# Optimization experiments

Measured on AMD Instinct MI355X. Metric: run time of the kernel, lower is better.

The kernel has to match this reference:

```python
import jax, jax.numpy as jnp
import numpy as np

DIM = 512
HEADS = 16
GRID = (32, 32)
MLP_HIDDEN = 2048
EPS = 1e-5


def _relative_position_index(hw):
    H, W = hw
    coords = np.stack(np.meshgrid(np.arange(H), np.arange(W), indexing='ij'))  # [2,H,W]
    coords = coords.reshape(2, -1)  # [2, L]
    rel = coords[:, :, None] - coords[:, None, :]  # [2, L, L]
    rel = rel.transpose(1, 2, 0).astype(np.int64)  # [L, L, 2]
    rel[:, :, 0] += H - 1
    rel[:, :, 1] += W - 1
    rel[:, :, 0] *= 2 * W - 1
    return jnp.asarray(rel.sum(-1))  # [L, L]


def setup_inputs() -> dict:
    key = jax.random.key(0)
    ks = jax.random.split(key, 12)
    L = GRID[0] * GRID[1]
    table_size = (2 * GRID[0] - 1) * (2 * GRID[1] - 1)
    s = 0.02
    return {
        'x': jax.random.normal(ks[0], (8, L, DIM), jnp.float32),
        'rel_index': _relative_position_index(GRID),
        'bias_table': s * jax.random.truncated_normal(ks[1], -2.0, 2.0, (table_size, HEADS), jnp.float32),
        'qkv_w': jax.random.normal(ks[2], (DIM, 3 * DIM), jnp.float32) / np.sqrt(DIM),
        'qkv_b': jnp.zeros((3 * DIM,), jnp.float32),
        'proj_w': jax.random.normal(ks[3], (DIM, DIM), jnp.float32) / np.sqrt(DIM),
        'proj_b': jnp.zeros((DIM,), jnp.float32),
        'n1_g': jnp.ones((DIM,), jnp.float32),
        'n1_b': jnp.zeros((DIM,), jnp.float32),
        'n2_g': jnp.ones((DIM,), jnp.float32),
        'n2_b': jnp.zeros((DIM,), jnp.float32),
        'fc1_w': jax.random.normal(ks[4], (DIM, MLP_HIDDEN), jnp.float32) / np.sqrt(DIM),
        'fc1_b': jnp.zeros((MLP_HIDDEN,), jnp.float32),
        'fc2_w': jax.random.normal(ks[5], (MLP_HIDDEN, DIM), jnp.float32) / np.sqrt(MLP_HIDDEN),
        'fc2_b': jnp.zeros((DIM,), jnp.float32),
    }


def _layernorm(x, g, b):
    mu = jnp.mean(x, -1, keepdims=True)
    var = jnp.mean(jnp.square(x - mu), -1, keepdims=True)
    return (x - mu) * jax.lax.rsqrt(var + EPS) * g + b


def reference(x, rel_index, bias_table, qkv_w, qkv_b, proj_w, proj_b,
              n1_g, n1_b, n2_g, n2_b, fc1_w, fc1_b, fc2_w, fc2_b):
    B, L, C = x.shape
    hd = C // HEADS
    scale = hd ** -0.5

    h = _layernorm(x, n1_g, n1_b)
    qkv = (h @ qkv_w + qkv_b).reshape(B, L, 3, HEADS, hd)
    qkv = jnp.transpose(qkv, (2, 0, 3, 1, 4))  # [3, B, H, L, hd]
    q, k, v = qkv[0] * scale, qkv[1], qkv[2]

    attn = jnp.einsum('bhld,bhmd->bhlm', q, k)  # [B, H, L, L]
    bias = bias_table[rel_index]                # [L, L, H]
    attn = attn + jnp.transpose(bias, (2, 0, 1))[None]
    attn = jax.nn.softmax(attn, axis=-1)

    out = jnp.einsum('bhlm,bhmd->bhld', attn, v)
    out = jnp.transpose(out, (0, 2, 1, 3)).reshape(B, L, C)
    out = out @ proj_w + proj_b

    x = x + out
    h2 = _layernorm(x, n2_g, n2_b)
    mlp = jax.nn.gelu(h2 @ fc1_w + fc1_b, approximate=False) @ fc2_w + fc2_b
    return x + mlp
```

## Files before the change

### kernel.cpp

```cpp
#include <hip/hip_runtime.h>

typedef unsigned short u16;
typedef __attribute__((ext_vector_type(8))) short bf16x8;
typedef __attribute__((ext_vector_type(4))) float f32x4;

__device__ __forceinline__ float bf2f(unsigned int u) {
    union { unsigned int i; float f; } c; c.i = u << 16; return c.f;
}
__device__ __forceinline__ unsigned int f2bf(float f) {
    union { float f; unsigned int i; } c; c.f = f;
    unsigned int x = c.i;
    unsigned int r = x + 0x7FFFu + ((x >> 16) & 1u);
    return r >> 16;
}

__device__ __forceinline__ void gload_lds16(const u16* g, u16* l) {
    __builtin_amdgcn_global_load_lds(
        (__attribute__((address_space(1))) void*)const_cast<u16*>(g),
        (__attribute__((address_space(3))) void*)l,
        16, 0, 0);
}

__global__ __launch_bounds__(256) void wconv_kernel(const float* __restrict__ W,
                                                    u16* __restrict__ Wt, int K, int N) {
    __shared__ u16 tile[32][36];
    int k0 = blockIdx.y * 32, n0 = blockIdx.x * 32;
    int t = threadIdx.x;
    int r = t >> 3, c4 = (t & 7) * 4;
    float4 v = *(const float4*)(W + (size_t)(k0 + r) * N + n0 + c4);
    tile[r][c4 + 0] = (u16)f2bf(v.x);
    tile[r][c4 + 1] = (u16)f2bf(v.y);
    tile[r][c4 + 2] = (u16)f2bf(v.z);
    tile[r][c4 + 3] = (u16)f2bf(v.w);
    __syncthreads();
    int n = t >> 3, k4 = (t & 7) * 4;
    u16 a0 = tile[k4 + 0][n], a1 = tile[k4 + 1][n];
    u16 a2 = tile[k4 + 2][n], a3 = tile[k4 + 3][n];
    uint2 st;
    st.x = (unsigned)a0 | ((unsigned)a1 << 16);
    st.y = (unsigned)a2 | ((unsigned)a3 << 16);
    *(uint2*)(Wt + (size_t)(n0 + n) * K + k0 + k4) = st;
}

__global__ __launch_bounds__(256) void ln_kernel(const float* __restrict__ x,
                                                 const float* __restrict__ g,
                                                 const float* __restrict__ b,
                                                 u16* __restrict__ y) {
    int row = blockIdx.x * 4 + (threadIdx.x >> 6);
    int t = threadIdx.x & 63;
    const float* xr = x + (size_t)row * 512 + t * 8;
    float4 a = *(const float4*)xr;
    float4 c = *(const float4*)(xr + 4);
    float v[8] = { a.x, a.y, a.z, a.w, c.x, c.y, c.z, c.w };
    float s = 0.f, ss = 0.f;
#pragma unroll
    for (int i = 0; i < 8; ++i) { s += v[i]; ss += v[i] * v[i]; }
#pragma unroll
    for (int off = 32; off; off >>= 1) {
        s  += __shfl_down(s, off);
        ss += __shfl_down(ss, off);
    }
    s = __shfl(s, 0); ss = __shfl(ss, 0);
    float mu = s * (1.0f / 512.0f);
    float var = ss * (1.0f / 512.0f) - mu * mu;
    float r = rsqrtf(var + 1e-5f);
    float4 g0 = *(const float4*)(g + t * 8);
    float4 g1 = *(const float4*)(g + t * 8 + 4);
    float4 b0 = *(const float4*)(b + t * 8);
    float4 b1 = *(const float4*)(b + t * 8 + 4);
    float gv[8] = { g0.x, g0.y, g0.z, g0.w, g1.x, g1.y, g1.z, g1.w };
    float bv[8] = { b0.x, b0.y, b0.z, b0.w, b1.x, b1.y, b1.z, b1.w };
    unsigned int o[4];
#pragma unroll
    for (int i = 0; i < 4; ++i) {
        float o0 = (v[2 * i] - mu) * r * gv[2 * i] + bv[2 * i];
        float o1 = (v[2 * i + 1] - mu) * r * gv[2 * i + 1] + bv[2 * i + 1];
        o[i] = f2bf(o0) | (f2bf(o1) << 16);
    }
    *(uint4*)(y + (size_t)row * 512 + t * 8) = make_uint4(o[0], o[1], o[2], o[3]);
}

template <int ACT, int RES, int COUT>
__global__ __launch_bounds__(256) void gemm_mfma(const u16* __restrict__ A, int lda,
                                                 const u16* __restrict__ Bt,
                                                 const float* __restrict__ bias,
                                                 const float* __restrict__ res, int ldres,
                                                 void* __restrict__ C, int ldC, int K,
                                                 int gx) {
    __shared__ u16 As[2][2][64 * 32];
    __shared__ u16 Bs[2][2][128 * 32];
    int tid = threadIdx.x;
    int G = gridDim.x;
    int bid = blockIdx.x;
    int wg = (bid & 7) * (G >> 3) + (bid >> 3);
    int bm = (wg / gx) * 64, bn = (wg % gx) * 128;
    int lane = tid & 63, wv = tid >> 6;
    int q = lane >> 4, lr = lane & 15;
    int wr = wv >> 1, wc = wv & 1;

    const u16* Ag = A + (size_t)(bm + wv * 16 + (lane >> 2)) * lda + (lane & 3) * 8;
    const u16* Bg = Bt + (size_t)(bn + wv * 32 + (lane >> 2)) * K + (lane & 3) * 8;
    int aoff  = (wv * 16) * 32;
    int boff0 = (wv * 32) * 32;
    int boff1 = (wv * 32 + 16) * 32;
    int apf = (wr * 32 + lr) * 32 + q * 8;
    int bpf = (wc * 64 + lr) * 32 + q * 8;

    f32x4 acc[2][4];
#pragma unroll
    for (int i = 0; i < 2; ++i)
#pragma unroll
        for (int j = 0; j < 4; ++j) acc[i][j] = (f32x4){0.f, 0.f, 0.f, 0.f};

#pragma unroll
    for (int p = 0; p < 2; ++p) {
        gload_lds16(Ag + p * 32, &As[0][p][aoff]);
        gload_lds16(Bg + p * 32, &Bs[0][p][boff0]);
        gload_lds16(Bg + (size_t)16 * K + p * 32, &Bs[0][p][boff1]);
    }
    __syncthreads();

    int cur = 0;
    for (int k0 = 0; k0 < K; k0 += 64) {
        int nxt = cur ^ 1;
        if (k0 + 64 < K) {
#pragma unroll
            for (int p = 0; p < 2; ++p) {
                gload_lds16(Ag + k0 + 64 + p * 32, &As[nxt][p][aoff]);
                gload_lds16(Bg + k0 + 64 + p * 32, &Bs[nxt][p][boff0]);
                gload_lds16(Bg + (size_t)16 * K + k0 + 64 + p * 32, &Bs[nxt][p][boff1]);
            }
        }
#pragma unroll
        for (int p = 0; p < 2; ++p) {
            bf16x8 af[2], bfr[4];
#pragma unroll
            for (int i = 0; i < 2; ++i) af[i] = *(const bf16x8*)&As[cur][p][apf + i * 16 * 32];
#pragma unroll
            for (int j = 0; j < 4; ++j) bfr[j] = *(const bf16x8*)&Bs[cur][p][bpf + j * 16 * 32];
#pragma unroll
            for (int i = 0; i < 2; ++i)
#pragma unroll
                for (int j = 0; j < 4; ++j)
                    acc[i][j] = __builtin_amdgcn_mfma_f32_16x16x32_bf16(af[i], bfr[j], acc[i][j], 0, 0, 0);
        }
        __syncthreads();
        cur = nxt;
    }

    float bv[4];
#pragma unroll
    for (int j = 0; j < 4; ++j)
        bv[j] = bias ? bias[bn + wc * 64 + j * 16 + lr] : 0.f;
#pragma unroll
    for (int i = 0; i < 2; ++i) {
#pragma unroll
        for (int j = 0; j < 4; ++j) {
            int col = bn + wc * 64 + j * 16 + lr;
#pragma unroll
            for (int r = 0; r < 4; ++r) {
                int row = bm + wr * 32 + i * 16 + q * 4 + r;
                float v = acc[i][j][r] + bv[j];
                if (ACT) v = 0.5f * v * (1.0f + erff(v * 0.7071067811865475f));
                if (RES) v += res[(size_t)row * ldres + col];
                if (COUT == 0) ((u16*)C)[(size_t)row * ldC + col] = (u16)f2bf(v);
                else           ((float*)C)[(size_t)row * ldC + col] = v;
            }
        }
    }
}

__global__ __launch_bounds__(256) void attn_mfma(u16* __restrict__ qkv,
                                                 const float* __restrict__ bias_table) {
    __shared__ u16 Ks[128][40];
    __shared__ u16 Vt[32][136];
    __shared__ u16 Ps[4][16][136];
    __shared__ float biasc[3969];
    int tid = threadIdx.x;
    int bid = blockIdx.x;
    int grp = (bid & 7) * 8 + ((bid >> 3) >> 4);
    int qt = (bid >> 3) & 15;
    int h = grp & 15, z = grp >> 4;
    u16* qkvz = qkv + (size_t)z * 1024 * 1536;

    for (int i = tid; i < 3969; i += 256) biasc[i] = bias_table[(size_t)i * 16 + h];

    int lane = tid & 63, wv = tid >> 6;
    int q = lane >> 4, m = lane & 15;

    int qrow = qt * 64 + wv * 16 + m;
    bf16x8 qf = *(const bf16x8*)(qkvz + (size_t)qrow * 1536 + h * 32 + q * 8);

    int arow[4];
#pragma unroll
    for (int r = 0; r < 4; ++r) {
        int l = qt * 64 + wv * 16 + q * 4 + r;
        arow[r] = (l >> 5) * 63 + (l & 31) + 1984;
    }

    const float scale = 0.17677669529663687f;
    float mrow[4] = { -1e30f, -1e30f, -1e30f, -1e30f };
    float lrow[4] = { 0.f, 0.f, 0.f, 0.f };
    f32x4 acco[2] = { (f32x4){0.f,0.f,0.f,0.f}, (f32x4){0.f,0.f,0.f,0.f} };

    int key = tid >> 1, dh = (tid & 1) * 16;
    const u16* kvsrc = qkvz + (size_t)key * 1536 + 512 + h * 32 + dh;
    uint4 pk0, pk1, pv0, pv1;
    pk0 = *(const uint4*)(kvsrc);
    pk1 = *(const uint4*)(kvsrc + 8);
    pv0 = *(const uint4*)(kvsrc + 512);
    pv1 = *(const uint4*)(kvsrc + 520);

    for (int kt = 0; kt < 8; ++kt) {
        __syncthreads();
        *(uint4*)&Ks[key][dh] = pk0;
        *(uint4*)&Ks[key][dh + 8] = pk1;
        {
            u16 tmp[16];
            *(uint4*)tmp = pv0; *(uint4*)(tmp + 8) = pv1;
#pragma unroll
            for (int j = 0; j < 16; ++j) Vt[dh + j][key] = tmp[j];
        }
        __syncthreads();
        if (kt < 7) {
            const u16* src = kvsrc + (size_t)(kt + 1) * 128 * 1536;
            pk0 = *(const uint4*)(src);
            pk1 = *(const uint4*)(src + 8);
            pv0 = *(const uint4*)(src + 512);
            pv1 = *(const uint4*)(src + 520);
        }

        f32x4 s8[8];
#pragma unroll
        for (int t = 0; t < 8; ++t) {
            bf16x8 kf = *(const bf16x8*)&Ks[t * 16 + m][q * 8];
            s8[t] = __builtin_amdgcn_mfma_f32_16x16x32_bf16(
                qf, kf, (f32x4){0.f,0.f,0.f,0.f}, 0, 0, 0);
        }
#pragma unroll
        for (int t = 0; t < 8; ++t) {
            int bb = (kt * 4 + (t >> 1)) * 63 + (t & 1) * 16 + m;
#pragma unroll
            for (int r = 0; r < 4; ++r)
                s8[t][r] = s8[t][r] * scale + biasc[arow[r] - bb];
        }
        float alpha[4];
#pragma unroll
        for (int r = 0; r < 4; ++r) {
            float v = s8[0][r];
#pragma unroll
            for (int t = 1; t < 8; ++t) v = fmaxf(v, s8[t][r]);
            v = fmaxf(v, __shfl_xor(v, 1));
            v = fmaxf(v, __shfl_xor(v, 2));
            v = fmaxf(v, __shfl_xor(v, 4));
            v = fmaxf(v, __shfl_xor(v, 8));
            float mn = fmaxf(mrow[r], v);
            alpha[r] = __expf(mrow[r] - mn);
            mrow[r] = mn;
            float sum = 0.f;
#pragma unroll
            for (int t = 0; t < 8; ++t) {
                float p = __expf(s8[t][r] - mn);
                s8[t][r] = p;
                sum += p;
            }
            sum += __shfl_xor(sum, 1);
            sum += __shfl_xor(sum, 2);
            sum += __shfl_xor(sum, 4);
            sum += __shfl_xor(sum, 8);
            lrow[r] = lrow[r] * alpha[r] + sum;
        }
#pragma unroll
        for (int t = 0; t < 8; ++t)
#pragma unroll
            for (int r = 0; r < 4; ++r)
                Ps[wv][q * 4 + r][t * 16 + m] = (u16)f2bf(s8[t][r]);
#pragma unroll
        for (int dt = 0; dt < 2; ++dt)
#pragma unroll
            for (int r = 0; r < 4; ++r) acco[dt][r] *= alpha[r];
#pragma unroll
        for (int c = 0; c < 4; ++c) {
            bf16x8 pf = *(const bf16x8*)&Ps[wv][m][c * 32 + q * 8];
#pragma unroll
            for (int dt = 0; dt < 2; ++dt) {
                bf16x8 vf = *(const bf16x8*)&Vt[dt * 16 + m][c * 32 + q * 8];
                acco[dt] = __builtin_amdgcn_mfma_f32_16x16x32_bf16(pf, vf, acco[dt], 0, 0, 0);
            }
        }
    }
#pragma unroll
    for (int r = 0; r < 4; ++r) {
        int l = qt * 64 + wv * 16 + q * 4 + r;
        float inv = 1.0f / lrow[r];
#pragma unroll
        for (int dt = 0; dt < 2; ++dt)
            qkvz[(size_t)l * 1536 + h * 32 + dt * 16 + m] = (u16)f2bf(acco[dt][r] * inv);
    }
}

extern "C" void kernel_launch(void* const* d_in, const int* in_sizes, int n_in,
                              void* d_out, int out_size, void* d_ws, size_t ws_size,
                              hipStream_t stream) {
    const float* x          = (const float*)d_in[0];
    const float* bias_table = (const float*)d_in[2];
    const float* qkv_w      = (const float*)d_in[3];
    const float* qkv_b      = (const float*)d_in[4];
    const float* proj_w     = (const float*)d_in[5];
    const float* proj_b     = (const float*)d_in[6];
    const float* n1g        = (const float*)d_in[7];
    const float* n1b        = (const float*)d_in[8];
    const float* n2g        = (const float*)d_in[9];
    const float* n2b        = (const float*)d_in[10];
    const float* fc1_w      = (const float*)d_in[11];
    const float* fc1_b      = (const float*)d_in[12];
    const float* fc2_w      = (const float*)d_in[13];
    const float* fc2_b      = (const float*)d_in[14];
    float* out = (float*)d_out;

    u16* ws16 = (u16*)d_ws;
    u16* wq_t = ws16;
    u16* wp_t = ws16 + 786432;
    u16* w1_t = ws16 + 1048576;
    u16* w2_t = ws16 + 2097152;
    u16* h    = ws16 + 3145728;
    u16* qkvb = ws16 + 7340032;
    u16* hid  = qkvb;

    wconv_kernel<<<dim3(48, 16), 256, 0, stream>>>(qkv_w, wq_t, 512, 1536);
    wconv_kernel<<<dim3(16, 16), 256, 0, stream>>>(proj_w, wp_t, 512, 512);
    wconv_kernel<<<dim3(64, 16), 256, 0, stream>>>(fc1_w, w1_t, 512, 2048);
    wconv_kernel<<<dim3(16, 64), 256, 0, stream>>>(fc2_w, w2_t, 2048, 512);

    ln_kernel<<<2048, 256, 0, stream>>>(x, n1g, n1b, h);

    for (int half = 0; half < 2; ++half) {
        size_t ro = (size_t)half * 4096;
        gemm_mfma<0, 0, 0><<<dim3(768), 256, 0, stream>>>(
            h + ro * 512, 512, wq_t, qkv_b, nullptr, 0, qkvb, 1536, 512, 12);
        attn_mfma<<<dim3(1024), 256, 0, stream>>>(qkvb, bias_table);
        gemm_mfma<0, 1, 1><<<dim3(256), 256, 0, stream>>>(
            qkvb, 1536, wp_t, proj_b, x + ro * 512, 512, out + ro * 512, 512, 512, 4);
    }

    ln_kernel<<<2048, 256, 0, stream>>>(out, n2g, n2b, h);

    for (int half = 0; half < 2; ++half) {
        size_t ro = (size_t)half * 4096;
        gemm_mfma<1, 0, 0><<<dim3(1024), 256, 0, stream>>>(
            h + ro * 512, 512, w1_t, fc1_b, nullptr, 0, hid, 2048, 512, 16);
        gemm_mfma<0, 1, 1><<<dim3(256), 256, 0, stream>>>(
            hid, 2048, w2_t, fc2_b, out + ro * 512, 512, out + ro * 512, 512, 2048, 4);
    }
}
```

Before: 374.8 us.

## Use triple-buffered K-loop in GEMM and load only needed bias-table slice in attention

```diff
diff --git a/kernel.cpp b/kernel.cpp
--- a/kernel.cpp
+++ b/kernel.cpp
@@ -87,8 +87,8 @@
                                                  const float* __restrict__ res, int ldres,
                                                  void* __restrict__ C, int ldC, int K,
                                                  int gx) {
-    __shared__ u16 As[2][2][64 * 32];
-    __shared__ u16 Bs[2][2][128 * 32];
+    __shared__ u16 As[3][64 * 32];
+    __shared__ u16 Bs[3][128 * 32];
     int tid = threadIdx.x;
     int G = gridDim.x;
     int bid = blockIdx.x;
@@ -106,46 +106,49 @@
     int apf = (wr * 32 + lr) * 32 + q * 8;
     int bpf = (wc * 64 + lr) * 32 + q * 8;
 
+    auto issue = [&](int t, int b) {
+        int k0 = t << 5;
+        gload_lds16(Ag + k0, &As[b][aoff]);
+        gload_lds16(Bg + k0, &Bs[b][boff0]);
+        gload_lds16(Bg + (size_t)16 * K + k0, &Bs[b][boff1]);
+    };
+
     f32x4 acc[2][4];
 #pragma unroll
     for (int i = 0; i < 2; ++i)
 #pragma unroll
         for (int j = 0; j < 4; ++j) acc[i][j] = (f32x4){0.f, 0.f, 0.f, 0.f};
 
-#pragma unroll
-    for (int p = 0; p < 2; ++p) {
-        gload_lds16(Ag + p * 32, &As[0][p][aoff]);
-        gload_lds16(Bg + p * 32, &Bs[0][p][boff0]);
-        gload_lds16(Bg + (size_t)16 * K + p * 32, &Bs[0][p][boff1]);
-    }
-    __syncthreads();
-
-    int cur = 0;
-    for (int k0 = 0; k0 < K; k0 += 64) {
-        int nxt = cur ^ 1;
-        if (k0 + 64 < K) {
-#pragma unroll
-            for (int p = 0; p < 2; ++p) {
-                gload_lds16(Ag + k0 + 64 + p * 32, &As[nxt][p][aoff]);
-                gload_lds16(Bg + k0 + 64 + p * 32, &Bs[nxt][p][boff0]);
-                gload_lds16(Bg + (size_t)16 * K + k0 + 64 + p * 32, &Bs[nxt][p][boff1]);
-            }
-        }
-#pragma unroll
-        for (int p = 0; p < 2; ++p) {
-            bf16x8 af[2], bfr[4];
-#pragma unroll
-            for (int i = 0; i < 2; ++i) af[i] = *(const bf16x8*)&As[cur][p][apf + i * 16 * 32];
-#pragma unroll
-            for (int j = 0; j < 4; ++j) bfr[j] = *(const bf16x8*)&Bs[cur][p][bpf + j * 16 * 32];
-#pragma unroll
-            for (int i = 0; i < 2; ++i)
-#pragma unroll
-                for (int j = 0; j < 4; ++j)
-                    acc[i][j] = __builtin_amdgcn_mfma_f32_16x16x32_bf16(af[i], bfr[j], acc[i][j], 0, 0, 0);
-        }
-        __syncthreads();
-        cur = nxt;
+    int T = K >> 5;
+    issue(0, 0);
+    issue(1, 1);
+    asm volatile("s_waitcnt vmcnt(3)" ::: "memory");
+    __builtin_amdgcn_s_barrier();
+    __builtin_amdgcn_sched_barrier(0);
+
+    int bc = 0, bp = 2;
+    for (int t = 0; t < T; ++t) {
+        if (t + 2 < T) issue(t + 2, bp);
+        bf16x8 af[2], bfr[4];
+#pragma unroll
+        for (int i = 0; i < 2; ++i) af[i] = *(const bf16x8*)&As[bc][apf + i * 16 * 32];
+#pragma unroll
+        for (int j = 0; j < 4; ++j) bfr[j] = *(const bf16x8*)&Bs[bc][bpf + j * 16 * 32];
+#pragma unroll
+        for (int i = 0; i < 2; ++i)
+#pragma unroll
+            for (int j = 0; j < 4; ++j)
+                acc[i][j] = __builtin_amdgcn_mfma_f32_16x16x32_bf16(af[i], bfr[j], acc[i][j], 0, 0, 0);
+        if (t + 1 < T) {
+            if (t + 2 < T)
+                asm volatile("s_waitcnt vmcnt(3) lgkmcnt(0)" ::: "memory");
+            else
+                asm volatile("s_waitcnt vmcnt(0) lgkmcnt(0)" ::: "memory");
+            __builtin_amdgcn_s_barrier();
+            __builtin_amdgcn_sched_barrier(0);
+        }
+        bc = (bc == 2) ? 0 : bc + 1;
+        bp = (bp == 2) ? 0 : bp + 1;
     }
 
     float bv[4];
@@ -175,7 +178,7 @@
     __shared__ u16 Ks[128][40];
     __shared__ u16 Vt[32][136];
     __shared__ u16 Ps[4][16][136];
-    __shared__ float biasc[3969];
+    __shared__ float biasc[2112];
     int tid = threadIdx.x;
     int bid = blockIdx.x;
     int grp = (bid & 7) * 8 + ((bid >> 3) >> 4);
@@ -183,7 +186,11 @@
     int h = grp & 15, z = grp >> 4;
     u16* qkvz = qkv + (size_t)z * 1024 * 1536;
 
-    for (int i = tid; i < 3969; i += 256) biasc[i] = bias_table[(size_t)i * 16 + h];
+    int bbase = qt * 126;
+    for (int i = tid; i < 2112; i += 256) {
+        int gi = bbase + i;
+        if (gi < 3969) biasc[i] = bias_table[(size_t)gi * 16 + h];
+    }
 
     int lane = tid & 63, wv = tid >> 6;
     int q = lane >> 4, m = lane & 15;
@@ -194,8 +201,8 @@
     int arow[4];
 #pragma unroll
     for (int r = 0; r < 4; ++r) {
-        int l = qt * 64 + wv * 16 + q * 4 + r;
-        arow[r] = (l >> 5) * 63 + (l & 31) + 1984;
+        int inner = wv * 16 + q * 4 + r;
+        arow[r] = (inner >> 5) * 63 + (inner & 31) + 1984;
     }
 
     const float scale = 0.17677669529663687f;
```

After: 380.2 us. No clear change (+1.4%).

## Use 64-wide N tiles for projection GEMMs and cache only needed bias slice

Applied to the files above, without the earlier changes.

```diff
diff --git a/kernel.cpp b/kernel.cpp
--- a/kernel.cpp
+++ b/kernel.cpp
@@ -80,43 +80,45 @@
     *(uint4*)(y + (size_t)row * 512 + t * 8) = make_uint4(o[0], o[1], o[2], o[3]);
 }
 
-template <int ACT, int RES, int COUT>
+template <int ACT, int RES, int COUT, int BN>
 __global__ __launch_bounds__(256) void gemm_mfma(const u16* __restrict__ A, int lda,
                                                  const u16* __restrict__ Bt,
                                                  const float* __restrict__ bias,
                                                  const float* __restrict__ res, int ldres,
                                                  void* __restrict__ C, int ldC, int K,
                                                  int gx) {
+    constexpr int JN = BN / 32;
     __shared__ u16 As[2][2][64 * 32];
-    __shared__ u16 Bs[2][2][128 * 32];
+    __shared__ u16 Bs[2][2][BN * 32];
     int tid = threadIdx.x;
     int G = gridDim.x;
     int bid = blockIdx.x;
     int wg = (bid & 7) * (G >> 3) + (bid >> 3);
-    int bm = (wg / gx) * 64, bn = (wg % gx) * 128;
+    int bm = (wg / gx) * 64, bn = (wg % gx) * BN;
     int lane = tid & 63, wv = tid >> 6;
     int q = lane >> 4, lr = lane & 15;
     int wr = wv >> 1, wc = wv & 1;
 
     const u16* Ag = A + (size_t)(bm + wv * 16 + (lane >> 2)) * lda + (lane & 3) * 8;
-    const u16* Bg = Bt + (size_t)(bn + wv * 32 + (lane >> 2)) * K + (lane & 3) * 8;
+    const u16* Bg = Bt + (size_t)(bn + wv * (BN / 4) + (lane >> 2)) * K + (lane & 3) * 8;
     int aoff  = (wv * 16) * 32;
-    int boff0 = (wv * 32) * 32;
-    int boff1 = (wv * 32 + 16) * 32;
+    int boff0 = (wv * (BN / 4)) * 32;
+    int boff1 = (wv * (BN / 4) + 16) * 32;
     int apf = (wr * 32 + lr) * 32 + q * 8;
-    int bpf = (wc * 64 + lr) * 32 + q * 8;
-
-    f32x4 acc[2][4];
+    int bpf = (wc * (BN / 2) + lr) * 32 + q * 8;
+
+    f32x4 acc[2][JN];
 #pragma unroll
     for (int i = 0; i < 2; ++i)
 #pragma unroll
-        for (int j = 0; j < 4; ++j) acc[i][j] = (f32x4){0.f, 0.f, 0.f, 0.f};
+        for (int j = 0; j < JN; ++j) acc[i][j] = (f32x4){0.f, 0.f, 0.f, 0.f};
 
 #pragma unroll
     for (int p = 0; p < 2; ++p) {
         gload_lds16(Ag + p * 32, &As[0][p][aoff]);
         gload_lds16(Bg + p * 32, &Bs[0][p][boff0]);
-        gload_lds16(Bg + (size_t)16 * K + p * 32, &Bs[0][p][boff1]);
+        if constexpr (BN == 128)
+            gload_lds16(Bg + (size_t)16 * K + p * 32, &Bs[0][p][boff1]);
     }
     __syncthreads();
 
@@ -128,35 +130,36 @@
             for (int p = 0; p < 2; ++p) {
                 gload_lds16(Ag + k0 + 64 + p * 32, &As[nxt][p][aoff]);
                 gload_lds16(Bg + k0 + 64 + p * 32, &Bs[nxt][p][boff0]);
-                gload_lds16(Bg + (size_t)16 * K + k0 + 64 + p * 32, &Bs[nxt][p][boff1]);
+                if constexpr (BN == 128)
+                    gload_lds16(Bg + (size_t)16 * K + k0 + 64 + p * 32, &Bs[nxt][p][boff1]);
             }
         }
 #pragma unroll
         for (int p = 0; p < 2; ++p) {
-            bf16x8 af[2], bfr[4];
+            bf16x8 af[2], bfr[JN];
 #pragma unroll
             for (int i = 0; i < 2; ++i) af[i] = *(const bf16x8*)&As[cur][p][apf + i * 16 * 32];
 #pragma unroll
-            for (int j = 0; j < 4; ++j) bfr[j] = *(const bf16x8*)&Bs[cur][p][bpf + j * 16 * 32];
+            for (int j = 0; j < JN; ++j) bfr[j] = *(const bf16x8*)&Bs[cur][p][bpf + j * 16 * 32];
 #pragma unroll
             for (int i = 0; i < 2; ++i)
 #pragma unroll
-                for (int j = 0; j < 4; ++j)
+                for (int j = 0; j < JN; ++j)
                     acc[i][j] = __builtin_amdgcn_mfma_f32_16x16x32_bf16(af[i], bfr[j], acc[i][j], 0, 0, 0);
         }
         __syncthreads();
         cur = nxt;
     }
 
-    float bv[4];
-#pragma unroll
-    for (int j = 0; j < 4; ++j)
-        bv[j] = bias ? bias[bn + wc * 64 + j * 16 + lr] : 0.f;
+    float bv[JN];
+#pragma unroll
+    for (int j = 0; j < JN; ++j)
+        bv[j] = bias ? bias[bn + wc * (BN / 2) + j * 16 + lr] : 0.f;
 #pragma unroll
     for (int i = 0; i < 2; ++i) {
 #pragma unroll
-        for (int j = 0; j < 4; ++j) {
-            int col = bn + wc * 64 + j * 16 + lr;
+        for (int j = 0; j < JN; ++j) {
+            int col = bn + wc * (BN / 2) + j * 16 + lr;
 #pragma unroll
             for (int r = 0; r < 4; ++r) {
                 int row = bm + wr * 32 + i * 16 + q * 4 + r;
@@ -175,7 +178,7 @@
     __shared__ u16 Ks[128][40];
     __shared__ u16 Vt[32][136];
     __shared__ u16 Ps[4][16][136];
-    __shared__ float biasc[3969];
+    __shared__ float biasc[2112];
     int tid = threadIdx.x;
     int bid = blockIdx.x;
     int grp = (bid & 7) * 8 + ((bid >> 3) >> 4);
@@ -183,7 +186,11 @@
     int h = grp & 15, z = grp >> 4;
     u16* qkvz = qkv + (size_t)z * 1024 * 1536;
 
-    for (int i = tid; i < 3969; i += 256) biasc[i] = bias_table[(size_t)i * 16 + h];
+    int bbase = qt * 126;
+    for (int i = tid; i < 2112; i += 256) {
+        int gi = bbase + i;
+        if (gi < 3969) biasc[i] = bias_table[(size_t)gi * 16 + h];
+    }
 
     int lane = tid & 63, wv = tid >> 6;
     int q = lane >> 4, m = lane & 15;
@@ -194,8 +201,8 @@
     int arow[4];
 #pragma unroll
     for (int r = 0; r < 4; ++r) {
-        int l = qt * 64 + wv * 16 + q * 4 + r;
-        arow[r] = (l >> 5) * 63 + (l & 31) + 1984;
+        int inner = wv * 16 + q * 4 + r;
+        arow[r] = (inner >> 5) * 63 + (inner & 31) + 1984;
     }
 
     const float scale = 0.17677669529663687f;
@@ -336,20 +343,20 @@
 
     for (int half = 0; half < 2; ++half) {
         size_t ro = (size_t)half * 4096;
-        gemm_mfma<0, 0, 0><<<dim3(768), 256, 0, stream>>>(
+        gemm_mfma<0, 0, 0, 128><<<dim3(768), 256, 0, stream>>>(
             h + ro * 512, 512, wq_t, qkv_b, nullptr, 0, qkvb, 1536, 512, 12);
         attn_mfma<<<dim3(1024), 256, 0, stream>>>(qkvb, bias_table);
-        gemm_mfma<0, 1, 1><<<dim3(256), 256, 0, stream>>>(
-            qkvb, 1536, wp_t, proj_b, x + ro * 512, 512, out + ro * 512, 512, 512, 4);
+        gemm_mfma<0, 1, 1, 64><<<dim3(512), 256, 0, stream>>>(
+            qkvb, 1536, wp_t, proj_b, x + ro * 512, 512, out + ro * 512, 512, 512, 8);
     }
 
     ln_kernel<<<2048, 256, 0, stream>>>(out, n2g, n2b, h);
 
     for (int half = 0; half < 2; ++half) {
         size_t ro = (size_t)half * 4096;
-        gemm_mfma<1, 0, 0><<<dim3(1024), 256, 0, stream>>>(
+        gemm_mfma<1, 0, 0, 128><<<dim3(1024), 256, 0, stream>>>(
             h + ro * 512, 512, w1_t, fc1_b, nullptr, 0, hid, 2048, 512, 16);
-        gemm_mfma<0, 1, 1><<<dim3(256), 256, 0, stream>>>(
-            hid, 2048, w2_t, fc2_b, out + ro * 512, 512, out + ro * 512, 512, 2048, 4);
-    }
-}
+        gemm_mfma<0, 1, 1, 64><<<dim3(512), 256, 0, stream>>>(
+            hid, 2048, w2_t, fc2_b, out + ro * 512, 512, out + ro * 512, 512, 2048, 8);
+    }
+}
```

Measured after the change: 355.2 us. 1.06x faster.
